# Kernel tuning notes

Measured on AMD Instinct MI355X. Metric: run time of the kernel, lower is better.

The kernel has to match this reference:

```python
import jax, jax.numpy as jnp
import numpy as np

N_NODES = 50000
N_EDGES = 1600000
IN_DIM = 128
N_HEADS = 8
OUT_DIM = 16  # output_dim // n_heads = 128 // 8


def setup_inputs() -> dict:
    key = jax.random.key(0)
    ks = jax.random.split(key, 8)
    feature = jax.random.normal(ks[0], (N_NODES, IN_DIM), dtype=jnp.float32)
    edge_src = jax.random.randint(ks[1], (N_EDGES,), 0, N_NODES)
    edge_dst = jax.random.randint(ks[2], (N_EDGES,), 0, N_NODES)
    edge_weight = jax.random.uniform(ks[3], (N_EDGES,), dtype=jnp.float32)
    w_lin = jax.random.normal(ks[4], (IN_DIM, N_HEADS * OUT_DIM), dtype=jnp.float32) * 0.1
    att_l = jax.random.normal(ks[5], (N_HEADS, OUT_DIM), dtype=jnp.float32) * 0.1
    att_r = jax.random.normal(ks[6], (N_HEADS, OUT_DIM), dtype=jnp.float32) * 0.1
    w_res = jax.random.normal(ks[7], (IN_DIM, N_HEADS * OUT_DIM), dtype=jnp.float32) * 0.1
    return {"feature": feature, "edge_src": edge_src, "edge_dst": edge_dst,
            "edge_weight": edge_weight, "w_lin": w_lin, "att_l": att_l,
            "att_r": att_r, "w_res": w_res}


def reference(feature, edge_src, edge_dst, edge_weight, w_lin, att_l, att_r, w_res):
    N = feature.shape[0]
    H, C = att_l.shape
    # Linear projection -> [N, H, C]
    x = (feature @ w_lin).reshape(N, H, C)
    # Per-node attention logits [N, H]
    al = jnp.einsum('nhc,hc->nh', x, att_l)
    ar = jnp.einsum('nhc,hc->nh', x, att_r)
    # Per-edge logits: gather src/dst, weight, leaky-relu  [E, H]
    alpha = al[edge_src] + ar[edge_dst]
    alpha = edge_weight[:, None] * alpha
    alpha = jax.nn.leaky_relu(alpha, negative_slope=0.2)
    # Segment softmax over edges grouped by destination node
    m = jax.ops.segment_max(alpha, edge_dst, num_segments=N)  # [N, H]
    m = jnp.where(jnp.isfinite(m), m, 0.0)
    e = jnp.exp(alpha - m[edge_dst])
    denom = jax.ops.segment_sum(e, edge_dst, num_segments=N)  # [N, H]
    coef = e / denom[edge_dst]                                 # [E, H]
    # Message passing: gather src feats, weight by coef, scatter-sum to dst
    msg = x[edge_src] * coef[:, :, None]                       # [E, H, C]
    feat = jax.ops.segment_sum(msg, edge_dst, num_segments=N)  # [N, H, C]
    out = jax.nn.elu(feat).reshape(N, H * C)
    out = out + feature @ w_res  # residual branch
    return out
```

## Files before the change

kernel.cpp:

```cpp
#include <hip/hip_runtime.h>
#include <math.h>

#define IN_DIM 128
#define NH 8
#define OC 16
#define HC 128
#define BSTR 136
#define ECH 4096
#define NBINS_MAX 512
#define FSTR 132

typedef __attribute__((ext_vector_type(8))) short short8;
typedef __attribute__((ext_vector_type(4))) float f32x4;

__device__ __forceinline__ unsigned short bf16_rne(float f) {
  unsigned int u = __builtin_bit_cast(unsigned int, f);
  u += 0x7FFFu + ((u >> 16) & 1u);
  return (unsigned short)(u >> 16);
}
__device__ __forceinline__ float bf16_to_f(unsigned short h) {
  unsigned int u = ((unsigned int)h) << 16;
  return __builtin_bit_cast(float, u);
}

__global__ __launch_bounds__(256) void k1_fused(const float* __restrict__ feature,
                                                const float* __restrict__ w_lin,
                                                const float* __restrict__ w_res,
                                                const float* __restrict__ att_l,
                                                const float* __restrict__ att_r,
                                                unsigned char* __restrict__ x8,
                                                float* __restrict__ sscale,
                                                float* __restrict__ al,
                                                float* __restrict__ ar,
                                                float* __restrict__ out,
                                                int* __restrict__ bin_cursor, int N) {
  __shared__ unsigned short BL[HC * BSTR];
  __shared__ unsigned short BR[HC * BSTR];
  const int t = threadIdx.x;
  if (blockIdx.x == 0) {
    bin_cursor[t] = 0;
    bin_cursor[t + 256] = 0;
  }
  for (int i = t; i < IN_DIM * HC; i += 256) {
    const int r = i >> 7, c = i & 127;
    BL[c * BSTR + r] = bf16_rne(w_lin[i]);
    BR[c * BSTR + r] = bf16_rne(w_res[i]);
  }
  __syncthreads();

  const int wave = t >> 6, lane = t & 63;
  const int n16 = lane & 15, quad = lane >> 4;
  float attl[8], attr[8];
#pragma unroll
  for (int hh = 0; hh < 8; ++hh) {
    attl[hh] = att_l[hh * OC + n16];
    attr[hh] = att_r[hh * OC + n16];
  }
  const int nStrips = (N + 15) >> 4;

  for (int strip = blockIdx.x * 4 + wave; strip < nStrips; strip += gridDim.x * 4) {
    const int row0 = strip * 16;
    const int arow = row0 + n16;
    const float* __restrict__ ap =
        feature + (size_t)((arow < N) ? arow : 0) * IN_DIM + quad * 8;
    short8 ahi[4], alo[4];
#pragma unroll
    for (int ks = 0; ks < 4; ++ks) {
      const float4 f0 = *(const float4*)(ap + ks * 32);
      const float4 f1 = *(const float4*)(ap + ks * 32 + 4);
      const float fv[8] = {f0.x, f0.y, f0.z, f0.w, f1.x, f1.y, f1.z, f1.w};
      short8 h, l;
#pragma unroll
      for (int j = 0; j < 8; ++j) {
        const unsigned short hh = bf16_rne(fv[j]);
        h[j] = (short)hh;
        l[j] = (short)bf16_rne(fv[j] - bf16_to_f(hh));
      }
      ahi[ks] = h;
      alo[ks] = l;
    }
    f32x4 xacc[8];
#pragma unroll
    for (int u = 0; u < 8; ++u) xacc[u] = (f32x4){0.f, 0.f, 0.f, 0.f};
#pragma unroll
    for (int ks = 0; ks < 4; ++ks) {
#pragma unroll
      for (int u = 0; u < 8; ++u) {
        const int boff = (u * 16 + n16) * BSTR + ks * 32 + quad * 8;
        const short8 bh = *(const short8*)&BL[boff];
        xacc[u] = __builtin_amdgcn_mfma_f32_16x16x32_bf16(ahi[ks], bh, xacc[u], 0, 0, 0);
        xacc[u] = __builtin_amdgcn_mfma_f32_16x16x32_bf16(alo[ks], bh, xacc[u], 0, 0, 0);
      }
    }
    float m[4];
#pragma unroll
    for (int r = 0; r < 4; ++r) {
      float mm = 0.f;
#pragma unroll
      for (int u = 0; u < 8; ++u) mm = fmaxf(mm, fabsf(xacc[u][r]));
      mm = fmaxf(mm, __shfl_xor(mm, 1));
      mm = fmaxf(mm, __shfl_xor(mm, 2));
      mm = fmaxf(mm, __shfl_xor(mm, 4));
      mm = fmaxf(mm, __shfl_xor(mm, 8));
      m[r] = mm;
    }
#pragma unroll
    for (int r = 0; r < 4; ++r) {
      const int rr = row0 + quad * 4 + r;
      if (rr < N) {
        const float inv = (m[r] > 0.f) ? 127.f / m[r] : 0.f;
#pragma unroll
        for (int u = 0; u < 8; ++u) {
          const int q8 = (int)rintf(xacc[u][r] * inv) + 128;
          x8[(size_t)rr * HC + u * 16 + n16] = (unsigned char)q8;
        }
        if (n16 == 0) sscale[rr] = (m[r] > 0.f) ? m[r] / 127.f : 0.f;
      }
    }
#pragma unroll
    for (int u = 0; u < 8; ++u) {
#pragma unroll
      for (int r = 0; r < 4; ++r) {
        float tl = xacc[u][r] * attl[u];
        float tr = xacc[u][r] * attr[u];
        tl += __shfl_xor(tl, 1);
        tr += __shfl_xor(tr, 1);
        tl += __shfl_xor(tl, 2);
        tr += __shfl_xor(tr, 2);
        tl += __shfl_xor(tl, 4);
        tr += __shfl_xor(tr, 4);
        tl += __shfl_xor(tl, 8);
        tr += __shfl_xor(tr, 8);
        const int rr = row0 + quad * 4 + r;
        if (n16 == 0 && rr < N) {
          al[(size_t)rr * NH + u] = tl;
          ar[(size_t)rr * NH + u] = tr;
        }
      }
    }
#pragma unroll
    for (int cg = 0; cg < 2; ++cg) {
      f32x4 acc[4] = {{0.f,0.f,0.f,0.f},{0.f,0.f,0.f,0.f},{0.f,0.f,0.f,0.f},{0.f,0.f,0.f,0.f}};
#pragma unroll
      for (int ks = 0; ks < 4; ++ks) {
#pragma unroll
        for (int j = 0; j < 4; ++j) {
          const int boff = ((cg * 4 + j) * 16 + n16) * BSTR + ks * 32 + quad * 8;
          const short8 bh = *(const short8*)&BR[boff];
          acc[j] = __builtin_amdgcn_mfma_f32_16x16x32_bf16(ahi[ks], bh, acc[j], 0, 0, 0);
          acc[j] = __builtin_amdgcn_mfma_f32_16x16x32_bf16(alo[ks], bh, acc[j], 0, 0, 0);
        }
      }
#pragma unroll
      for (int j = 0; j < 4; ++j) {
        const int colo = (cg * 4 + j) * 16 + n16;
#pragma unroll
        for (int r = 0; r < 4; ++r) {
          const int rr = row0 + quad * 4 + r;
          if (rr < N) out[(size_t)rr * HC + colo] = acc[j][r];
        }
      }
    }
  }
}

__global__ __launch_bounds__(256) void kb1_scatter(const int* __restrict__ esrc,
                                                   const int* __restrict__ edst,
                                                   const float* __restrict__ ew,
                                                   int* __restrict__ bin_cursor,
                                                   uint2* __restrict__ tmp,
                                                   int E, int nbins, int cap) {
  __shared__ int cnt[NBINS_MAX];
  __shared__ int gbase[NBINS_MAX];
  const int t = threadIdx.x;
  cnt[t] = 0;
  cnt[t + 256] = 0;
  __syncthreads();
  const int base = blockIdx.x * ECH;
  uint2 v[16];
  int bj[16], sj[16];
#pragma unroll
  for (int j = 0; j < 16; ++j) {
    const int e = base + j * 256 + t;
    bj[j] = -1;
    if (e < E) {
      const int d = edst[e];
      v[j] = make_uint2((unsigned)esrc[e] | ((unsigned)(d & 127) << 16),
                        __float_as_uint(ew[e]));
      bj[j] = d >> 7;
      sj[j] = atomicAdd(&cnt[bj[j]], 1);
    }
  }
  __syncthreads();
  for (int b = t; b < nbins; b += 256) {
    const int own = cnt[b];
    if (own > 0) gbase[b] = atomicAdd(&bin_cursor[b], own);
  }
  __syncthreads();
#pragma unroll
  for (int j = 0; j < 16; ++j)
    if (bj[j] >= 0) {
      const int p = gbase[bj[j]] + sj[j];
      if (p >= 0 && p < cap) tmp[(size_t)bj[j] * cap + p] = v[j];
    }
}

__global__ __launch_bounds__(256) void kb3_sort(const uint2* __restrict__ tmp,
                                                const int* __restrict__ bin_cursor,
                                                uint2* __restrict__ packed,
                                                int* __restrict__ row_start,
                                                int cap, int nbins, int N) {
  const int b = blockIdx.x, t = threadIdx.x;
  const int M = bin_cursor[b];
  __shared__ int redw[4];
  int part = 0;
  for (int i = t; i < b; i += 256) part += bin_cursor[i];
#pragma unroll
  for (int o = 32; o >= 1; o >>= 1) part += __shfl_xor(part, o);
  if ((t & 63) == 0) redw[t >> 6] = part;
  __syncthreads();
  const int gstart = redw[0] + redw[1] + redw[2] + redw[3];
  if (b == nbins - 1 && t == 0) row_start[N] = gstart + M;

  const uint2* __restrict__ src = tmp + (size_t)b * cap;
  __shared__ int cnt[128];
  __shared__ int cur[128];
  __shared__ int s[128];
  if (t < 128) cnt[t] = 0;
  __syncthreads();
  for (int i = t; i < M; i += 256) atomicAdd(&cnt[src[i].x >> 16], 1);
  __syncthreads();
  if (t < 128) s[t] = cnt[t];
  __syncthreads();
  for (int o = 1; o < 128; o <<= 1) {
    int a = 0;
    if (t < 128 && t >= o) a = s[t - o];
    __syncthreads();
    if (t < 128) s[t] += a;
    __syncthreads();
  }
  if (t < 128) {
    const int ex = s[t] - cnt[t];
    cur[t] = gstart + ex;
    const int node = b * 128 + t;
    if (node < N) row_start[node] = gstart + ex;
  }
  __syncthreads();
  for (int i = t; i < M; i += 256) {
    const uint2 v = src[i];
    const int pos = atomicAdd(&cur[v.x >> 16], 1);
    packed[pos] = make_uint2(v.x & 0xFFFFu, v.y);
  }
}

__global__ __launch_bounds__(64) void k5_agg(const unsigned char* __restrict__ x8,
                                             const float* __restrict__ s,
                                             const uint2* __restrict__ packed,
                                             const int* __restrict__ row_start,
                                             const float* __restrict__ al,
                                             const float* __restrict__ ar,
                                             float* __restrict__ out, int N) {
  const int n = blockIdx.x;
  const int l = threadIdx.x;
  const int s0 = row_start[n];
  const int En = row_start[n + 1] - s0;
  if (En == 0) return;
  __shared__ int sbuf[64];
  __shared__ float wbuf[64];
  __shared__ float scbuf[64];
  __shared__ float fred[8 * FSTR];
  const int h = l & 7;
  const int g = l >> 3;
  const int ch0 = h * 16;

  const float arn = ar[(size_t)n * NH + h];
  float dpart = 0.f;
  float facsum = 0.f;
  float f[16];
#pragma unroll
  for (int j = 0; j < 16; ++j) f[j] = 0.f;

  for (int base = 0; base < En; base += 64) {
    const int cnt = min(64, En - base);
    __syncthreads();
    if (l < cnt) {
      const uint2 p = packed[s0 + base + l];
      const int src = (int)p.x;
      sbuf[l] = src;
      wbuf[l] = __uint_as_float(p.y);
      scbuf[l] = s[src];
    }
    __syncthreads();
    for (int i = g; i < cnt; i += 8) {
      const int src = sbuf[i];
      float a = wbuf[i] * (al[(size_t)src * NH + h] + arn);
      a = (a > 0.f) ? a : 0.2f * a;
      const float e = __expf(a);
      dpart += e;
      const float fac = e * scbuf[i];
      facsum += fac;
      const int4 qw = *(const int4*)(x8 + (size_t)src * HC + ch0);
      const unsigned ux = (unsigned)qw.x, uy = (unsigned)qw.y;
      const unsigned uz = (unsigned)qw.z, uw = (unsigned)qw.w;
      f[0]  = fmaf(fac, (float)(ux & 0xFFu),         f[0]);
      f[1]  = fmaf(fac, (float)((ux >> 8) & 0xFFu),  f[1]);
      f[2]  = fmaf(fac, (float)((ux >> 16) & 0xFFu), f[2]);
      f[3]  = fmaf(fac, (float)(ux >> 24),           f[3]);
      f[4]  = fmaf(fac, (float)(uy & 0xFFu),         f[4]);
      f[5]  = fmaf(fac, (float)((uy >> 8) & 0xFFu),  f[5]);
      f[6]  = fmaf(fac, (float)((uy >> 16) & 0xFFu), f[6]);
      f[7]  = fmaf(fac, (float)(uy >> 24),           f[7]);
      f[8]  = fmaf(fac, (float)(uz & 0xFFu),         f[8]);
      f[9]  = fmaf(fac, (float)((uz >> 8) & 0xFFu),  f[9]);
      f[10] = fmaf(fac, (float)((uz >> 16) & 0xFFu), f[10]);
      f[11] = fmaf(fac, (float)(uz >> 24),           f[11]);
      f[12] = fmaf(fac, (float)(uw & 0xFFu),         f[12]);
      f[13] = fmaf(fac, (float)((uw >> 8) & 0xFFu),  f[13]);
      f[14] = fmaf(fac, (float)((uw >> 16) & 0xFFu), f[14]);
      f[15] = fmaf(fac, (float)(uw >> 24),           f[15]);
    }
  }
  dpart += __shfl_xor(dpart, 8);
  dpart += __shfl_xor(dpart, 16);
  dpart += __shfl_xor(dpart, 32);
  facsum += __shfl_xor(facsum, 8);
  facsum += __shfl_xor(facsum, 16);
  facsum += __shfl_xor(facsum, 32);
#pragma unroll
  for (int q = 0; q < 4; ++q) {
    const f32x4 v = {f[q * 4 + 0], f[q * 4 + 1], f[q * 4 + 2], f[q * 4 + 3]};
    *(f32x4*)&fred[g * FSTR + ch0 + q * 4] = v;
  }
  __syncthreads();
  float a0 = 0.f, a1 = 0.f;
#pragma unroll
  for (int gg = 0; gg < 8; ++gg) {
    const float2 v = *(const float2*)&fred[gg * FSTR + 2 * l];
    a0 += v.x;
    a1 += v.y;
  }
  const float dH = __shfl(dpart, l >> 3);
  const float fsH = __shfl(facsum, l >> 3);
  const float inv = 1.f / dH;
  float f0 = (a0 - 128.f * fsH) * inv;
  float f1 = (a1 - 128.f * fsH) * inv;
  f0 = (f0 > 0.f) ? f0 : (__expf(f0) - 1.f);
  f1 = (f1 > 0.f) ? f1 : (__expf(f1) - 1.f);
  float2 o = *(float2*)&out[(size_t)n * HC + 2 * l];
  o.x += f0;
  o.y += f1;
  *(float2*)&out[(size_t)n * HC + 2 * l] = o;
}

extern "C" void kernel_launch(void* const* d_in, const int* in_sizes, int n_in,
                              void* d_out, int out_size, void* d_ws, size_t ws_size,
                              hipStream_t stream) {
  const float* feature = (const float*)d_in[0];
  const int* esrc = (const int*)d_in[1];
  const int* edst = (const int*)d_in[2];
  const float* ew = (const float*)d_in[3];
  const float* w_lin = (const float*)d_in[4];
  const float* att_l = (const float*)d_in[5];
  const float* att_r = (const float*)d_in[6];
  const float* w_res = (const float*)d_in[7];
  float* out = (float*)d_out;

  const int N = in_sizes[0] / IN_DIM;
  const int E = in_sizes[1];
  const int nbins = (N + 127) >> 7;
  int cap = (E + nbins - 1) / nbins;
  cap = cap + cap / 4 + 512;
  cap = (cap + 63) & ~63;
  const int nch = (E + ECH - 1) / ECH;

  char* ws = (char*)d_ws;
  size_t off = 0;
  auto alloc = [&](size_t bytes) {
    void* p = ws + off;
    off = (off + bytes + 255) & ~(size_t)255;
    return p;
  };
  uint2* tmp = (uint2*)alloc((size_t)nbins * cap * sizeof(uint2));
  unsigned char* x8 = (unsigned char*)alloc((size_t)N * HC);
  float* sscale = (float*)alloc((size_t)N * sizeof(float));
  float* al = (float*)alloc((size_t)N * NH * sizeof(float));
  float* ar = (float*)alloc((size_t)N * NH * sizeof(float));
  int* row_start = (int*)alloc((size_t)(N + 1) * sizeof(int));
  int* bin_cursor = (int*)alloc((size_t)NBINS_MAX * sizeof(int));
  uint2* packed = (uint2*)alloc((size_t)E * sizeof(uint2));

  k1_fused<<<512, 256, 0, stream>>>(feature, w_lin, w_res, att_l, att_r,
                                    x8, sscale, al, ar, out, bin_cursor, N);
  kb1_scatter<<<nch, 256, 0, stream>>>(esrc, edst, ew, bin_cursor, tmp, E, nbins, cap);
  kb3_sort<<<nbins, 256, 0, stream>>>(tmp, bin_cursor, packed, row_start, cap, nbins, N);
  k5_agg<<<N, 64, 0, stream>>>(x8, sscale, packed, row_start, al, ar, out, N);
}
```

Baseline: 204.0 us.

## Fold attention vectors into projection weights and widen scatter/sort blocks to 1024

Precomputes W_lin·att_l and W_lin·att_r per head into a small 16-column bf16 hi/lo matrix in shared memory. The per-node attention logits then come from a few extra MFMAs instead of long shuffle-reduction chains over the accumulators. Separately, the edge scatter and per-bin sort kernels move from 256 to 1024 threads per block, with per-thread edge counts adjusted to match. The folded weights change rounding slightly: the bf16 split is applied to the combined weights rather than to x. Larger blocks may also reduce occupancy or raise shared-memory atomic contention.

Result: faster. 193.3 us (-5.3%).

```diff
diff --git a/kernel.cpp b/kernel.cpp
--- a/kernel.cpp
+++ b/kernel.cpp
@@ -36,6 +36,8 @@
                                                 int* __restrict__ bin_cursor, int N) {
   __shared__ unsigned short BL[HC * BSTR];
   __shared__ unsigned short BR[HC * BSTR];
+  __shared__ unsigned short WH[16 * BSTR];
+  __shared__ unsigned short WL[16 * BSTR];
   const int t = threadIdx.x;
   if (blockIdx.x == 0) {
     bin_cursor[t] = 0;
@@ -46,16 +48,24 @@
     BL[c * BSTR + r] = bf16_rne(w_lin[i]);
     BR[c * BSTR + r] = bf16_rne(w_res[i]);
   }
+#pragma unroll
+  for (int j = 0; j < 8; ++j) {
+    const int idx = t * 8 + j;
+    const int k = idx >> 4, c = idx & 15;
+    const int h8 = c & 7;
+    const float* __restrict__ av = ((c < 8) ? att_l : att_r) + h8 * OC;
+    const float* __restrict__ wr = w_lin + k * HC + h8 * OC;
+    float acc = 0.f;
+#pragma unroll
+    for (int oc = 0; oc < 16; ++oc) acc = fmaf(wr[oc], av[oc], acc);
+    const unsigned short hi = bf16_rne(acc);
+    WH[c * BSTR + k] = hi;
+    WL[c * BSTR + k] = bf16_rne(acc - bf16_to_f(hi));
+  }
   __syncthreads();
 
   const int wave = t >> 6, lane = t & 63;
   const int n16 = lane & 15, quad = lane >> 4;
-  float attl[8], attr[8];
-#pragma unroll
-  for (int hh = 0; hh < 8; ++hh) {
-    attl[hh] = att_l[hh * OC + n16];
-    attr[hh] = att_r[hh * OC + n16];
-  }
   const int nStrips = (N + 15) >> 4;
 
   for (int strip = blockIdx.x * 4 + wave; strip < nStrips; strip += gridDim.x * 4) {
@@ -92,6 +102,26 @@
         xacc[u] = __builtin_amdgcn_mfma_f32_16x16x32_bf16(alo[ks], bh, xacc[u], 0, 0, 0);
       }
     }
+    {
+      f32x4 accA = {0.f, 0.f, 0.f, 0.f};
+#pragma unroll
+      for (int ks = 0; ks < 4; ++ks) {
+        const int boff = n16 * BSTR + ks * 32 + quad * 8;
+        const short8 wh = *(const short8*)&WH[boff];
+        const short8 wl = *(const short8*)&WL[boff];
+        accA = __builtin_amdgcn_mfma_f32_16x16x32_bf16(ahi[ks], wh, accA, 0, 0, 0);
+        accA = __builtin_amdgcn_mfma_f32_16x16x32_bf16(alo[ks], wh, accA, 0, 0, 0);
+        accA = __builtin_amdgcn_mfma_f32_16x16x32_bf16(ahi[ks], wl, accA, 0, 0, 0);
+      }
+#pragma unroll
+      for (int r = 0; r < 4; ++r) {
+        const int rr = row0 + quad * 4 + r;
+        if (rr < N) {
+          if (n16 < 8) al[(size_t)rr * NH + n16] = accA[r];
+          else         ar[(size_t)rr * NH + (n16 - 8)] = accA[r];
+        }
+      }
+    }
     float m[4];
 #pragma unroll
     for (int r = 0; r < 4; ++r) {
@@ -118,27 +148,6 @@
       }
     }
 #pragma unroll
-    for (int u = 0; u < 8; ++u) {
-#pragma unroll
-      for (int r = 0; r < 4; ++r) {
-        float tl = xacc[u][r] * attl[u];
-        float tr = xacc[u][r] * attr[u];
-        tl += __shfl_xor(tl, 1);
-        tr += __shfl_xor(tr, 1);
-        tl += __shfl_xor(tl, 2);
-        tr += __shfl_xor(tr, 2);
-        tl += __shfl_xor(tl, 4);
-        tr += __shfl_xor(tr, 4);
-        tl += __shfl_xor(tl, 8);
-        tr += __shfl_xor(tr, 8);
-        const int rr = row0 + quad * 4 + r;
-        if (n16 == 0 && rr < N) {
-          al[(size_t)rr * NH + u] = tl;
-          ar[(size_t)rr * NH + u] = tr;
-        }
-      }
-    }
-#pragma unroll
     for (int cg = 0; cg < 2; ++cg) {
       f32x4 acc[4] = {{0.f,0.f,0.f,0.f},{0.f,0.f,0.f,0.f},{0.f,0.f,0.f,0.f},{0.f,0.f,0.f,0.f}};
 #pragma unroll
@@ -164,24 +173,23 @@
   }
 }
 
-__global__ __launch_bounds__(256) void kb1_scatter(const int* __restrict__ esrc,
-                                                   const int* __restrict__ edst,
-                                                   const float* __restrict__ ew,
-                                                   int* __restrict__ bin_cursor,
-                                                   uint2* __restrict__ tmp,
-                                                   int E, int nbins, int cap) {
+__global__ __launch_bounds__(1024) void kb1_scatter(const int* __restrict__ esrc,
+                                                    const int* __restrict__ edst,
+                                                    const float* __restrict__ ew,
+                                                    int* __restrict__ bin_cursor,
+                                                    uint2* __restrict__ tmp,
+                                                    int E, int nbins, int cap) {
   __shared__ int cnt[NBINS_MAX];
   __shared__ int gbase[NBINS_MAX];
   const int t = threadIdx.x;
-  cnt[t] = 0;
-  cnt[t + 256] = 0;
+  if (t < NBINS_MAX) cnt[t] = 0;
   __syncthreads();
   const int base = blockIdx.x * ECH;
-  uint2 v[16];
-  int bj[16], sj[16];
-#pragma unroll
-  for (int j = 0; j < 16; ++j) {
-    const int e = base + j * 256 + t;
+  uint2 v[4];
+  int bj[4], sj[4];
+#pragma unroll
+  for (int j = 0; j < 4; ++j) {
+    const int e = base + j * 1024 + t;
     bj[j] = -1;
     if (e < E) {
       const int d = edst[e];
@@ -192,34 +200,36 @@
     }
   }
   __syncthreads();
-  for (int b = t; b < nbins; b += 256) {
+  for (int b = t; b < nbins; b += 1024) {
     const int own = cnt[b];
     if (own > 0) gbase[b] = atomicAdd(&bin_cursor[b], own);
   }
   __syncthreads();
 #pragma unroll
-  for (int j = 0; j < 16; ++j)
+  for (int j = 0; j < 4; ++j)
     if (bj[j] >= 0) {
       const int p = gbase[bj[j]] + sj[j];
       if (p >= 0 && p < cap) tmp[(size_t)bj[j] * cap + p] = v[j];
     }
 }
 
-__global__ __launch_bounds__(256) void kb3_sort(const uint2* __restrict__ tmp,
-                                                const int* __restrict__ bin_cursor,
-                                                uint2* __restrict__ packed,
-                                                int* __restrict__ row_start,
-                                                int cap, int nbins, int N) {
+__global__ __launch_bounds__(1024) void kb3_sort(const uint2* __restrict__ tmp,
+                                                 const int* __restrict__ bin_cursor,
+                                                 uint2* __restrict__ packed,
+                                                 int* __restrict__ row_start,
+                                                 int cap, int nbins, int N) {
   const int b = blockIdx.x, t = threadIdx.x;
   const int M = bin_cursor[b];
-  __shared__ int redw[4];
+  __shared__ int redw[16];
   int part = 0;
-  for (int i = t; i < b; i += 256) part += bin_cursor[i];
+  for (int i = t; i < b; i += 1024) part += bin_cursor[i];
 #pragma unroll
   for (int o = 32; o >= 1; o >>= 1) part += __shfl_xor(part, o);
   if ((t & 63) == 0) redw[t >> 6] = part;
   __syncthreads();
-  const int gstart = redw[0] + redw[1] + redw[2] + redw[3];
+  int gstart = 0;
+#pragma unroll
+  for (int w = 0; w < 16; ++w) gstart += redw[w];
   if (b == nbins - 1 && t == 0) row_start[N] = gstart + M;
 
   const uint2* __restrict__ src = tmp + (size_t)b * cap;
@@ -228,7 +238,7 @@
   __shared__ int s[128];
   if (t < 128) cnt[t] = 0;
   __syncthreads();
-  for (int i = t; i < M; i += 256) atomicAdd(&cnt[src[i].x >> 16], 1);
+  for (int i = t; i < M; i += 1024) atomicAdd(&cnt[src[i].x >> 16], 1);
   __syncthreads();
   if (t < 128) s[t] = cnt[t];
   __syncthreads();
@@ -246,7 +256,7 @@
     if (node < N) row_start[node] = gstart + ex;
   }
   __syncthreads();
-  for (int i = t; i < M; i += 256) {
+  for (int i = t; i < M; i += 1024) {
     const uint2 v = src[i];
     const int pos = atomicAdd(&cur[v.x >> 16], 1);
     packed[pos] = make_uint2(v.x & 0xFFFFu, v.y);
@@ -391,7 +401,7 @@
 
   k1_fused<<<512, 256, 0, stream>>>(feature, w_lin, w_res, att_l, att_r,
                                     x8, sscale, al, ar, out, bin_cursor, N);
-  kb1_scatter<<<nch, 256, 0, stream>>>(esrc, edst, ew, bin_cursor, tmp, E, nbins, cap);
-  kb3_sort<<<nbins, 256, 0, stream>>>(tmp, bin_cursor, packed, row_start, cap, nbins, N);
+  kb1_scatter<<<nch, 1024, 0, stream>>>(esrc, edst, ew, bin_cursor, tmp, E, nbins, cap);
+  kb3_sort<<<nbins, 1024, 0, stream>>>(tmp, bin_cursor, packed, row_start, cap, nbins, N);
   k5_agg<<<N, 64, 0, stream>>>(x8, sscale, packed, row_start, al, ar, out, N);
 }
```
